# Kernel optimization log

Measured on AMD Instinct MI355X. Metric: run time of the kernel, lower is better.

## Reference

```python
import jax, jax.numpy as jnp
import numpy as np

LAYERS = [2048, 2048, 2048, 512]
THRESHOLD = 1.0
TAU_MEM = 20.0
TAU_SYN = 5.0
DT = 1.0
BATCH = 32
T = 100


def setup_inputs() -> dict:
    key = jax.random.key(0)
    ks = jax.random.split(key, 2 + 2 * (len(LAYERS) - 1))
    inp = {
        "x": jax.random.uniform(ks[0], (BATCH, LAYERS[0]), dtype=jnp.float32),
        "noise": jax.random.uniform(ks[1], (T, BATCH, LAYERS[0]), dtype=jnp.float32),
        "time_steps": T,
    }
    # nn.Linear-style init: U(-1/sqrt(fan_in), 1/sqrt(fan_in))
    for i in range(len(LAYERS) - 1):
        fan_in, fan_out = LAYERS[i], LAYERS[i + 1]
        bound = 1.0 / np.sqrt(fan_in)
        inp[f"W{i}"] = jax.random.uniform(ks[2 + 2 * i], (fan_out, fan_in), minval=-bound, maxval=bound, dtype=jnp.float32)
        inp[f"b{i}"] = jax.random.uniform(ks[3 + 2 * i], (fan_out,), minval=-bound, maxval=bound, dtype=jnp.float32)
    return inp


def _lif_step(I, mem, syn):
    # dI_syn/dt = -I_syn/tau_syn + I ; dV/dt = -V/tau_mem + I_syn  (explicit Euler, dt=1)
    syn = syn + (-syn / TAU_SYN + I) * DT
    mem = mem + (-mem / TAU_MEM + syn) * DT
    spikes = (mem >= THRESHOLD).astype(mem.dtype)
    mem = mem * (1.0 - spikes)          # reset fired neurons
    mem = mem * (mem > 0).astype(mem.dtype)  # clamp negative potentials to 0
    return spikes, mem, syn


def reference(x, noise, W0, b0, W1, b1, W2, b2, time_steps):
    params = [(W0, b0), (W1, b1), (W2, b2)]
    batch = x.shape[0]
    dtype = x.dtype
    rate = jnp.clip(x, 0.0, 1.0)                       # [B, in]
    in_spikes = (noise < rate[None]).astype(dtype)     # [T, B, in] Poisson encoding

    mems = tuple(jnp.zeros((batch, W.shape[0]), dtype) for W, _ in params)
    syns = tuple(jnp.zeros((batch, W.shape[0]), dtype) for W, _ in params)

    def step(carry, sp_in):
        mems, syns = carry
        layer_in = sp_in
        new_mems, new_syns = [], []
        count = jnp.zeros((), dtype)
        for (W, b), m, s in zip(params, mems, syns):
            I = layer_in @ W.T + b
            spk, m, s = _lif_step(I, m, s)
            new_mems.append(m)
            new_syns.append(s)
            count = count + spk.sum()
            layer_in = spk
        return (tuple(new_mems), tuple(new_syns)), (layer_in, count)

    (_, _), (out_spikes, counts) = jax.lax.scan(step, (mems, syns), in_spikes)
    output = out_spikes.mean(axis=0)   # [B, out]: time-averaged output spike train
    total_spikes = counts.sum()
    return output, total_spikes
```

## Files before the change

kernel.cpp:

```cpp
#include <hip/hip_runtime.h>

#define T_STEPS 100
#define MTOT    3200
#define R0_OFF  0
#define R1_OFF  13107200
#define I_OFF   26214400

typedef _Float16 half8_t __attribute__((ext_vector_type(8)));
typedef _Float16 half4_t __attribute__((ext_vector_type(4)));
typedef float    f32x4   __attribute__((ext_vector_type(4)));

__device__ __forceinline__ void encode_body(
    int blk, const float* __restrict__ x, const float* __restrict__ noise,
    _Float16* __restrict__ spk0, float* __restrict__ out)
{
    if (blk == 0 && threadIdx.x == 0) out[16384] = 0.0f;
    const int tid = threadIdx.x;
    const int m0  = blk * 16;
    __shared__ half8_t lds[16 * 257];
    #pragma unroll
    for (int ml = 0; ml < 16; ++ml) {
        const int m = m0 + ml;
        const int t = m >> 5, b = m & 31;
        const float4 x1 = *(const float4*)(x + b * 2048 + tid * 8);
        const float4 x2 = *(const float4*)(x + b * 2048 + tid * 8 + 4);
        const float4 n1 = *(const float4*)(noise + (size_t)t * 65536 + b * 2048 + tid * 8);
        const float4 n2 = *(const float4*)(noise + (size_t)t * 65536 + b * 2048 + tid * 8 + 4);
        const float xr[8] = {x1.x,x1.y,x1.z,x1.w,x2.x,x2.y,x2.z,x2.w};
        const float nz[8] = {n1.x,n1.y,n1.z,n1.w,n2.x,n2.y,n2.z,n2.w};
        half8_t sp;
        #pragma unroll
        for (int j = 0; j < 8; ++j) {
            const float r = fminf(fmaxf(xr[j], 0.0f), 1.0f);
            sp[j] = (nz[j] < r) ? (_Float16)1.0f : (_Float16)0.0f;
        }
        lds[ml * 257 + tid] = sp;
    }
    __syncthreads();
    #pragma unroll
    for (int r = 0; r < 16; ++r) {
        const int ml  = tid & 15;
        const int oct = r * 16 + (tid >> 4);
        *(half8_t*)(spk0 + ((size_t)oct * MTOT + m0 + ml) * 8) = lds[ml * 257 + oct];
    }
}

__device__ __forceinline__ void convw_body(
    int blk, const float* __restrict__ W, _Float16* __restrict__ Wf)
{
    const int koct = threadIdx.x;
    #pragma unroll
    for (int r = 0; r < 8; ++r) {
        const int row = blk * 8 + r;
        const float* wp = W + (size_t)row * 2048 + koct * 8;
        const float4 f1 = *(const float4*)(wp);
        const float4 f2 = *(const float4*)(wp + 4);
        half8_t h = {(_Float16)f1.x,(_Float16)f1.y,(_Float16)f1.z,(_Float16)f1.w,
                     (_Float16)f2.x,(_Float16)f2.y,(_Float16)f2.z,(_Float16)f2.w};
        const size_t idx = (size_t)(row >> 4) * 32768
                         + ((size_t)((koct >> 2) * 64 + (koct & 3) * 16 + (row & 15))) * 8;
        *(half8_t*)(Wf + idx) = h;
    }
}

__device__ __forceinline__ void scan_body(
    int blk, const _Float16* __restrict__ I, const float* __restrict__ bias,
    _Float16* __restrict__ spk_out, float* __restrict__ out,
    const int nshift, const int is_last)
{
    const int gid = blk * 256 + threadIdx.x;
    const int j   = gid & 7;
    const int b   = (gid >> 3) & 31;
    const int oct = gid >> 8;
    const int n   = oct * 8 + j;
    const float bi = bias[n];
    const size_t nbase = (size_t)oct * (MTOT * 8) + j;
    float mem = 0.f, syn = 0.f, osum = 0.f, cnt = 0.f;
    #pragma unroll 4
    for (int t = 0; t < T_STEPS; ++t) {
        const int m = t * 32 + b;
        const float Iv = (float)I[nbase + (size_t)m * 8] + bi;
        syn = syn + (-syn / 5.0f + Iv);
        mem = mem + (-mem / 20.0f + syn);
        const float sv = (mem >= 1.0f) ? 1.0f : 0.0f;
        mem = (sv != 0.0f) ? 0.0f : mem;
        mem = (mem > 0.0f) ? mem : 0.0f;
        cnt += sv; osum += sv;
        if (!is_last) spk_out[nbase + (size_t)m * 8] = (_Float16)sv;
    }
    if (is_last) out[b * 512 + n] = osum * 0.01f;
    float c = cnt;
    #pragma unroll
    for (int s2 = 1; s2 < 64; s2 <<= 1) c += __shfl_xor(c, s2);
    if ((threadIdx.x & 63) == 0) atomicAdd(&out[16384], c);
    (void)nshift;
}

__global__ __launch_bounds__(256, 2) void snn_enc_convw_kernel(
    const float* __restrict__ x, const float* __restrict__ noise,
    _Float16* __restrict__ spk0, float* __restrict__ out,
    const float* __restrict__ W, _Float16* __restrict__ Wf)
{
    if (blockIdx.x < 200) encode_body(blockIdx.x, x, noise, spk0, out);
    else                  convw_body(blockIdx.x - 200, W, Wf);
}

__global__ __launch_bounds__(256, 4) void snn_scan_convw_kernel(
    const _Float16* __restrict__ I, const float* __restrict__ bias,
    _Float16* __restrict__ spk_out, float* __restrict__ out,
    const int scan_blocks, const int nshift,
    const float* __restrict__ W, _Float16* __restrict__ Wf)
{
    if ((int)blockIdx.x < scan_blocks)
        scan_body(blockIdx.x, I, bias, spk_out, out, nshift, 0);
    else
        convw_body(blockIdx.x - scan_blocks, W, Wf);
}

__global__ __launch_bounds__(256, 4) void snn_scan_kernel(
    const _Float16* __restrict__ I, const float* __restrict__ bias,
    float* __restrict__ out, const int nshift)
{
    scan_body(blockIdx.x, I, bias, nullptr, out, nshift, 1);
}


__device__ __forceinline__ half8_t ldB(const _Float16* __restrict__ p, int kq) {
    return *(const half8_t*)(p + (size_t)kq * (MTOT * 8));
}

__device__ __forceinline__ void stage_q(
    const _Float16* __restrict__ Wf, _Float16* __restrict__ wlds,
    const int nbb, const int q, const int w, const int lane)
{
    #pragma unroll
    for (int r = 0; r < 8; ++r) {
        const int unit = r * 512 + w * 64 + lane;
        const int s = unit >> 10, off = unit & 1023;
        const _Float16* src = Wf + (size_t)(4 * nbb + s) * 32768
                            + (size_t)q * 8192 + (size_t)off * 8;
        _Float16* dst = wlds + (size_t)unit * 8;
        __builtin_amdgcn_global_load_lds(
            (const __attribute__((address_space(1))) void*)src,
            (__attribute__((address_space(3))) void*)dst, 16, 0, 0);
    }
}

template<bool HAS2>
__device__ __forceinline__ void kstep512(
    const _Float16* __restrict__ wlds, const _Float16* const (&bp)[2],
    half8_t (&bb)[2], f32x4 (&acc)[2][4],
    const int lane, const int quad, const int kb, const int j)
{
    half8_t a[4];
    #pragma unroll
    for (int s = 0; s < 4; ++s)
        a[s] = *(const half8_t*)(wlds + (size_t)s * 8192 + (size_t)(j * 64 + lane) * 8);
    #pragma unroll
    for (int s = 0; s < 4; ++s) {
        acc[0][s] = __builtin_amdgcn_mfma_f32_16x16x32_f16(a[s], bb[0], acc[0][s], 0, 0, 0);
        if (HAS2)
            acc[1][s] = __builtin_amdgcn_mfma_f32_16x16x32_f16(a[s], bb[1], acc[1][s], 0, 0, 0);
    }
    if (kb + 2 < 64) {
        const int kq = (kb + 2) * 4 + quad;
        bb[0] = ldB(bp[0], kq);
        if (HAS2) bb[1] = ldB(bp[1], kq);
    }
}

template<bool HAS2>
__device__ __forceinline__ void gemm64s_run(
    const _Float16* __restrict__ Wf, const _Float16* __restrict__ spk,
    _Float16* __restrict__ I, _Float16* __restrict__ wlds,
    const int (&mt)[2], const int nbb, const int row_base,
    const int w, const int lane, const int quad, const int mi,
    const bool st)
{
    const _Float16* bp[2];
    bp[0] = spk + ((size_t)mt[0] * 16 + mi) * 8;
    bp[1] = spk + ((size_t)mt[1] * 16 + mi) * 8;

    half8_t bE[2], bO[2];
    bE[0] = ldB(bp[0], quad);
    bO[0] = ldB(bp[0], 4 + quad);
    if (HAS2) { bE[1] = ldB(bp[1], quad); bO[1] = ldB(bp[1], 4 + quad); }

    stage_q(Wf, wlds, nbb, 0, w, lane);
    __syncthreads();

    f32x4 acc[2][4];
    #pragma unroll
    for (int u = 0; u < 2; ++u) {
        #pragma unroll
        for (int s = 0; s < 4; ++s) acc[u][s] = (f32x4){0, 0, 0, 0};
    }

    #pragma unroll 1
    for (int q = 0; q < 4; ++q) {
        #pragma unroll
        for (int j = 0; j < 16; j += 2) {
            kstep512<HAS2>(wlds, bp, bE, acc, lane, quad, q * 16 + j,     j);
            kstep512<HAS2>(wlds, bp, bO, acc, lane, quad, q * 16 + j + 1, j + 1);
        }
        __syncthreads();
        if (q < 3) {
            stage_q(Wf, wlds, nbb, q + 1, w, lane);
            __syncthreads();
        }
    }

    #pragma unroll
    for (int s = 0; s < 4; ++s) {
        const int n0 = row_base + s * 16 + quad * 4;
        const size_t obase = (size_t)(n0 >> 3) * (MTOT * 8) + (n0 & 7);
        #pragma unroll
        for (int u = 0; u < 2; ++u) {
            if (u == 0 && !st) continue;
            if (u == 1 && !HAS2) continue;
            half4_t h;
            #pragma unroll
            for (int r = 0; r < 4; ++r) h[r] = (_Float16)acc[u][s][r];
            *(half4_t*)(I + obase + (size_t)(mt[u] * 16 + mi) * 8) = h;
        }
    }
}

template<int NCHUNK>
__global__ __launch_bounds__(512, 4) void snn_gemm64s_kernel(
    const _Float16* __restrict__ Wf, const _Float16* __restrict__ spk,
    _Float16* __restrict__ I)
{
    const int tid  = threadIdx.x;
    const int lane = tid & 63;
    const int w    = tid >> 6;
    const int mi   = lane & 15;
    const int quad = lane >> 4;
    const int chunk = blockIdx.x % NCHUNK;
    const int rest  = blockIdx.x / NCHUNK;
    const int msl   = rest & 1;
    const int nbb   = rest >> 1;
    const int row_base = nbb * 64;
    const int jt     = (200 - chunk + NCHUNK - 1) / NCHUNK;
    const int jh     = (jt + 1) >> 1;
    const int jbase  = msl ? jh : 0;
    const int jcount = msl ? (jt - jh) : jh;
    const int rem    = jcount - 8;
    const bool has2  = (w < rem);
    const int r2     = rem > 0 ? rem : 0;
    const bool st    = has2 || (w + r2) < jcount;
    int jl_start = jbase + (has2 ? 2 * w : w + r2);
    const int jmax = jbase + jcount - 1;
    if (jl_start > jmax) jl_start = jmax;

    int mt[2];
    #pragma unroll
    for (int u = 0; u < 2; ++u) {
        int jl = jl_start + u;
        if (jl > jmax) jl = jmax;
        mt[u] = chunk + NCHUNK * jl;
    }

    __shared__ _Float16 wlds[32768];

    if (has2) gemm64s_run<true >(Wf, spk, I, wlds, mt, nbb, row_base, w, lane, quad, mi, true);
    else      gemm64s_run<false>(Wf, spk, I, wlds, mt, nbb, row_base, w, lane, quad, mi, st);
}

extern "C" void kernel_launch(void* const* d_in, const int* in_sizes, int n_in,
                              void* d_out, int out_size, void* d_ws, size_t ws_size,
                              hipStream_t stream) {
    const float* x     = (const float*)d_in[0];
    const float* noise = (const float*)d_in[1];
    const float* W0 = (const float*)d_in[3];
    const float* b0 = (const float*)d_in[4];
    const float* W1 = (const float*)d_in[5];
    const float* b1 = (const float*)d_in[6];
    const float* W2 = (const float*)d_in[7];
    const float* b2 = (const float*)d_in[8];
    float* out = (float*)d_out;

    _Float16* R0 = (_Float16*)((char*)d_ws + R0_OFF);
    _Float16* R1 = (_Float16*)((char*)d_ws + R1_OFF);
    _Float16* Ib = (_Float16*)((char*)d_ws + I_OFF);

    snn_enc_convw_kernel<<<dim3(456), dim3(256), 0, stream>>>(x, noise, R0, out, W0, R1);
    snn_gemm64s_kernel<8><<<dim3(512), dim3(512), 0, stream>>>(R1, R0, Ib);
    snn_scan_convw_kernel<<<dim3(512), dim3(256), 0, stream>>>(Ib, b0, R1, out, 256, 11, W1, R0);
    snn_gemm64s_kernel<8><<<dim3(512), dim3(512), 0, stream>>>(R0, R1, Ib);
    snn_scan_convw_kernel<<<dim3(320), dim3(256), 0, stream>>>(Ib, b1, R0, out, 256, 11, W2, R1);
    snn_gemm64s_kernel<16><<<dim3(256), dim3(512), 0, stream>>>(R1, R0, Ib);
    snn_scan_kernel<<<dim3(64), dim3(256), 0, stream>>>(Ib, b2, out, 9);

    (void)in_sizes; (void)n_in; (void)out_size; (void)ws_size;
}
```

Measured before the change: 274.0 us.

## Fuse all stages into one cooperative persistent kernel with grid syncs

Merges encode, weight conversion, three GEMMs and three LIF scans into a single cooperative kernel launched with 512 blocks of 512 threads, separated by grid.sync barriers. It falls back to separate launches when occupancy allows fewer than two blocks per CU. The encode, convert and scan helpers are reworked for 512-thread blocks, and the encode LDS padding is replaced with an XOR swizzle. The goal is to remove the launch gaps and tails between the seven launches, at the cost of grid-barrier overhead and idle blocks during the small phases.

```diff
diff --git a/kernel.cpp b/kernel.cpp
--- a/kernel.cpp
+++ b/kernel.cpp
@@ -1,4 +1,5 @@
 #include <hip/hip_runtime.h>
+#include <hip/hip_cooperative_groups.h>
 
 #define T_STEPS 100
 #define MTOT    3200
@@ -10,48 +11,53 @@
 typedef _Float16 half4_t __attribute__((ext_vector_type(4)));
 typedef float    f32x4   __attribute__((ext_vector_type(4)));
 
-__device__ __forceinline__ void encode_body(
+__device__ __forceinline__ void encode512_body(
     int blk, const float* __restrict__ x, const float* __restrict__ noise,
-    _Float16* __restrict__ spk0, float* __restrict__ out)
+    _Float16* __restrict__ spk0, float* __restrict__ out, _Float16* smem)
 {
     if (blk == 0 && threadIdx.x == 0) out[16384] = 0.0f;
-    const int tid = threadIdx.x;
-    const int m0  = blk * 16;
-    __shared__ half8_t lds[16 * 257];
-    #pragma unroll
-    for (int ml = 0; ml < 16; ++ml) {
-        const int m = m0 + ml;
+    const int tid  = threadIdx.x;
+    const int m0   = blk * 16;
+    const int koct = tid & 255;
+    const int mlh  = tid >> 8;
+    half8_t* lds = (half8_t*)smem;
+    #pragma unroll
+    for (int mlq = 0; mlq < 8; ++mlq) {
+        const int ml = mlq * 2 + mlh;
+        const int m  = m0 + ml;
         const int t = m >> 5, b = m & 31;
-        const float4 x1 = *(const float4*)(x + b * 2048 + tid * 8);
-        const float4 x2 = *(const float4*)(x + b * 2048 + tid * 8 + 4);
-        const float4 n1 = *(const float4*)(noise + (size_t)t * 65536 + b * 2048 + tid * 8);
-        const float4 n2 = *(const float4*)(noise + (size_t)t * 65536 + b * 2048 + tid * 8 + 4);
+        const float4 x1 = *(const float4*)(x + b * 2048 + koct * 8);
+        const float4 x2 = *(const float4*)(x + b * 2048 + koct * 8 + 4);
+        const float4 n1 = *(const float4*)(noise + (size_t)t * 65536 + b * 2048 + koct * 8);
+        const float4 n2 = *(const float4*)(noise + (size_t)t * 65536 + b * 2048 + koct * 8 + 4);
         const float xr[8] = {x1.x,x1.y,x1.z,x1.w,x2.x,x2.y,x2.z,x2.w};
         const float nz[8] = {n1.x,n1.y,n1.z,n1.w,n2.x,n2.y,n2.z,n2.w};
         half8_t sp;
         #pragma unroll
-        for (int j = 0; j < 8; ++j) {
-            const float r = fminf(fmaxf(xr[j], 0.0f), 1.0f);
-            sp[j] = (nz[j] < r) ? (_Float16)1.0f : (_Float16)0.0f;
+        for (int q = 0; q < 8; ++q) {
+            const float r = fminf(fmaxf(xr[q], 0.0f), 1.0f);
+            sp[q] = (nz[q] < r) ? (_Float16)1.0f : (_Float16)0.0f;
         }
-        lds[ml * 257 + tid] = sp;
+        lds[ml * 256 + (koct ^ ml)] = sp;
     }
     __syncthreads();
     #pragma unroll
-    for (int r = 0; r < 16; ++r) {
+    for (int r = 0; r < 8; ++r) {
         const int ml  = tid & 15;
-        const int oct = r * 16 + (tid >> 4);
-        *(half8_t*)(spk0 + ((size_t)oct * MTOT + m0 + ml) * 8) = lds[ml * 257 + oct];
-    }
-}
-
-__device__ __forceinline__ void convw_body(
-    int blk, const float* __restrict__ W, _Float16* __restrict__ Wf)
-{
-    const int koct = threadIdx.x;
+        const int oct = r * 32 + (tid >> 4);
+        *(half8_t*)(spk0 + ((size_t)oct * MTOT + m0 + ml) * 8)
+            = lds[ml * 256 + (oct ^ ml)];
+    }
+}
+
+__device__ __forceinline__ void convw512_body(
+    int cblk, const float* __restrict__ W, _Float16* __restrict__ Wf)
+{
+    const int koct = threadIdx.x & 255;
+    const int rh   = threadIdx.x >> 8;
     #pragma unroll
     for (int r = 0; r < 8; ++r) {
-        const int row = blk * 8 + r;
+        const int row = cblk * 16 + rh * 8 + r;
         const float* wp = W + (size_t)row * 2048 + koct * 8;
         const float4 f1 = *(const float4*)(wp);
         const float4 f2 = *(const float4*)(wp + 4);
@@ -63,12 +69,11 @@
     }
 }
 
-__device__ __forceinline__ void scan_body(
+__device__ __forceinline__ void scan512_body(
     int blk, const _Float16* __restrict__ I, const float* __restrict__ bias,
-    _Float16* __restrict__ spk_out, float* __restrict__ out,
-    const int nshift, const int is_last)
-{
-    const int gid = blk * 256 + threadIdx.x;
+    _Float16* __restrict__ spk_out, float* __restrict__ out, const int is_last)
+{
+    const int gid = blk * 512 + threadIdx.x;
     const int j   = gid & 7;
     const int b   = (gid >> 3) & 31;
     const int oct = gid >> 8;
@@ -93,37 +98,7 @@
     #pragma unroll
     for (int s2 = 1; s2 < 64; s2 <<= 1) c += __shfl_xor(c, s2);
     if ((threadIdx.x & 63) == 0) atomicAdd(&out[16384], c);
-    (void)nshift;
-}
-
-__global__ __launch_bounds__(256, 2) void snn_enc_convw_kernel(
-    const float* __restrict__ x, const float* __restrict__ noise,
-    _Float16* __restrict__ spk0, float* __restrict__ out,
-    const float* __restrict__ W, _Float16* __restrict__ Wf)
-{
-    if (blockIdx.x < 200) encode_body(blockIdx.x, x, noise, spk0, out);
-    else                  convw_body(blockIdx.x - 200, W, Wf);
-}
-
-__global__ __launch_bounds__(256, 4) void snn_scan_convw_kernel(
-    const _Float16* __restrict__ I, const float* __restrict__ bias,
-    _Float16* __restrict__ spk_out, float* __restrict__ out,
-    const int scan_blocks, const int nshift,
-    const float* __restrict__ W, _Float16* __restrict__ Wf)
-{
-    if ((int)blockIdx.x < scan_blocks)
-        scan_body(blockIdx.x, I, bias, spk_out, out, nshift, 0);
-    else
-        convw_body(blockIdx.x - scan_blocks, W, Wf);
-}
-
-__global__ __launch_bounds__(256, 4) void snn_scan_kernel(
-    const _Float16* __restrict__ I, const float* __restrict__ bias,
-    float* __restrict__ out, const int nshift)
-{
-    scan_body(blockIdx.x, I, bias, nullptr, out, nshift, 1);
-}
-
+}
 
 __device__ __forceinline__ half8_t ldB(const _Float16* __restrict__ p, int kq) {
     return *(const half8_t*)(p + (size_t)kq * (MTOT * 8));
@@ -227,17 +202,18 @@
 }
 
 template<int NCHUNK>
-__global__ __launch_bounds__(512, 4) void snn_gemm64s_kernel(
-    const _Float16* __restrict__ Wf, const _Float16* __restrict__ spk,
-    _Float16* __restrict__ I)
+__device__ __forceinline__ void gemm64s_body(
+    const int bid, const _Float16* __restrict__ Wf,
+    const _Float16* __restrict__ spk, _Float16* __restrict__ I,
+    _Float16* __restrict__ wlds)
 {
     const int tid  = threadIdx.x;
     const int lane = tid & 63;
     const int w    = tid >> 6;
     const int mi   = lane & 15;
     const int quad = lane >> 4;
-    const int chunk = blockIdx.x % NCHUNK;
-    const int rest  = blockIdx.x / NCHUNK;
+    const int chunk = bid % NCHUNK;
+    const int rest  = bid / NCHUNK;
     const int msl   = rest & 1;
     const int nbb   = rest >> 1;
     const int row_base = nbb * 64;
@@ -261,10 +237,76 @@
         mt[u] = chunk + NCHUNK * jl;
     }
 
-    __shared__ _Float16 wlds[32768];
-
     if (has2) gemm64s_run<true >(Wf, spk, I, wlds, mt, nbb, row_base, w, lane, quad, mi, true);
     else      gemm64s_run<false>(Wf, spk, I, wlds, mt, nbb, row_base, w, lane, quad, mi, st);
+}
+
+__global__ __launch_bounds__(512, 4) void snn_mega_kernel(
+    const float* __restrict__ x, const float* __restrict__ noise,
+    const float* __restrict__ W0, const float* __restrict__ b0,
+    const float* __restrict__ W1, const float* __restrict__ b1,
+    const float* __restrict__ W2, const float* __restrict__ b2,
+    _Float16* __restrict__ R0, _Float16* __restrict__ R1,
+    _Float16* __restrict__ Ib, float* __restrict__ out)
+{
+    cooperative_groups::grid_group grid = cooperative_groups::this_grid();
+    __shared__ _Float16 smem[32768];
+    const int blk = blockIdx.x;
+
+    if (blk < 200)      encode512_body(blk, x, noise, R0, out, smem);
+    else if (blk < 328) convw512_body(blk - 200, W0, R1);
+    grid.sync();
+    gemm64s_body<8>(blk, R1, R0, Ib, smem);
+    grid.sync();
+    if (blk < 128)      scan512_body(blk, Ib, b0, R1, out, 0);
+    else if (blk < 256) convw512_body(blk - 128, W1, R0);
+    grid.sync();
+    gemm64s_body<8>(blk, R0, R1, Ib, smem);
+    grid.sync();
+    if (blk < 128)      scan512_body(blk, Ib, b1, R0, out, 0);
+    else if (blk < 160) convw512_body(blk - 128, W2, R1);
+    grid.sync();
+    if (blk < 256) gemm64s_body<16>(blk, R1, R0, Ib, smem);
+    grid.sync();
+    if (blk < 32) scan512_body(blk, Ib, b2, nullptr, out, 1);
+}
+
+__global__ __launch_bounds__(512, 4) void snn_enc512_kernel(
+    const float* __restrict__ x, const float* __restrict__ noise,
+    _Float16* __restrict__ spk0, float* __restrict__ out,
+    const float* __restrict__ W, _Float16* __restrict__ Wf)
+{
+    __shared__ _Float16 smem[32768];
+    if (blockIdx.x < 200) encode512_body(blockIdx.x, x, noise, spk0, out, smem);
+    else                  convw512_body(blockIdx.x - 200, W, Wf);
+}
+
+__global__ __launch_bounds__(512, 4) void snn_scan_convw512_kernel(
+    const _Float16* __restrict__ I, const float* __restrict__ bias,
+    _Float16* __restrict__ spk_out, float* __restrict__ out,
+    const int scan_blocks, const float* __restrict__ W,
+    _Float16* __restrict__ Wf)
+{
+    if ((int)blockIdx.x < scan_blocks)
+        scan512_body(blockIdx.x, I, bias, spk_out, out, 0);
+    else
+        convw512_body(blockIdx.x - scan_blocks, W, Wf);
+}
+
+__global__ __launch_bounds__(512, 4) void snn_scan512_kernel(
+    const _Float16* __restrict__ I, const float* __restrict__ bias,
+    float* __restrict__ out)
+{
+    scan512_body(blockIdx.x, I, bias, nullptr, out, 1);
+}
+
+template<int NCHUNK>
+__global__ __launch_bounds__(512, 4) void snn_gemm64s_kernel(
+    const _Float16* __restrict__ Wf, const _Float16* __restrict__ spk,
+    _Float16* __restrict__ I)
+{
+    __shared__ _Float16 wlds[32768];
+    gemm64s_body<NCHUNK>(blockIdx.x, Wf, spk, I, wlds);
 }
 
 extern "C" void kernel_launch(void* const* d_in, const int* in_sizes, int n_in,
@@ -284,13 +326,26 @@
     _Float16* R1 = (_Float16*)((char*)d_ws + R1_OFF);
     _Float16* Ib = (_Float16*)((char*)d_ws + I_OFF);
 
-    snn_enc_convw_kernel<<<dim3(456), dim3(256), 0, stream>>>(x, noise, R0, out, W0, R1);
-    snn_gemm64s_kernel<8><<<dim3(512), dim3(512), 0, stream>>>(R1, R0, Ib);
-    snn_scan_convw_kernel<<<dim3(512), dim3(256), 0, stream>>>(Ib, b0, R1, out, 256, 11, W1, R0);
-    snn_gemm64s_kernel<8><<<dim3(512), dim3(512), 0, stream>>>(R0, R1, Ib);
-    snn_scan_convw_kernel<<<dim3(320), dim3(256), 0, stream>>>(Ib, b1, R0, out, 256, 11, W2, R1);
-    snn_gemm64s_kernel<16><<<dim3(256), dim3(512), 0, stream>>>(R1, R0, Ib);
-    snn_scan_kernel<<<dim3(64), dim3(256), 0, stream>>>(Ib, b2, out, 9);
+    int maxb = 0;
+    hipError_t oe = hipOccupancyMaxActiveBlocksPerMultiprocessor(
+        &maxb, (const void*)snn_mega_kernel, 512, 0);
+
+    if (oe == hipSuccess && maxb >= 2) {
+        void* args[] = {(void*)&x, (void*)&noise,
+                        (void*)&W0, (void*)&b0, (void*)&W1, (void*)&b1,
+                        (void*)&W2, (void*)&b2,
+                        (void*)&R0, (void*)&R1, (void*)&Ib, (void*)&out};
+        hipLaunchCooperativeKernel((const void*)snn_mega_kernel,
+                                   dim3(512), dim3(512), args, 0, stream);
+    } else {
+        snn_enc512_kernel<<<dim3(328), dim3(512), 0, stream>>>(x, noise, R0, out, W0, R1);
+        snn_gemm64s_kernel<8><<<dim3(512), dim3(512), 0, stream>>>(R1, R0, Ib);
+        snn_scan_convw512_kernel<<<dim3(256), dim3(512), 0, stream>>>(Ib, b0, R1, out, 128, W1, R0);
+        snn_gemm64s_kernel<8><<<dim3(512), dim3(512), 0, stream>>>(R0, R1, Ib);
+        snn_scan_convw512_kernel<<<dim3(160), dim3(512), 0, stream>>>(Ib, b1, R0, out, 128, W2, R1);
+        snn_gemm64s_kernel<16><<<dim3(256), dim3(512), 0, stream>>>(R1, R0, Ib);
+        snn_scan512_kernel<<<dim3(32), dim3(512), 0, stream>>>(Ib, b2, out);
+    }
 
     (void)in_sizes; (void)n_in; (void)out_size; (void)ws_size;
 }
```

After: 273.4 us. Within noise of the previous version (-0.2%).
